# Kernel optimization log

Measured on AMD Instinct MI355X. Metric: run time of the kernel, lower is better.

Reference implementation:

```python
import jax, jax.numpy as jnp
import numpy as np
from jax import lax

M_DIM = 128
L1 = L2 = L3 = L4 = 4
L = L1 * L2 * L3 * L4  # 256
RANK = 2
BATCH, D = 4, 16
W = D - RANK + 1  # 15 windows per dim (linear mode, stride 1, drop)


def _make_bbasis():
    # Bbasis[idx, i] = prod_d cos(2*pi*(j_d+1)/(i+2)), idx = ((j1*L2+j2)*L3+j3)*L4+j4
    i = jnp.arange(M_DIM, dtype=jnp.float32)
    def c(Ld):
        j = jnp.arange(D_ := Ld, dtype=jnp.float32)
        return jnp.cos(2.0 * jnp.pi * (j[:, None] + 1.0) / (i[None, :] + 2.0))  # (Ld, m)
    B1, B2, B3, B4 = c(L1), c(L2), c(L3), c(L4)
    Bb = (B1[:, None, None, None, :] * B2[None, :, None, None, :]
          * B3[None, None, :, None, :] * B4[None, None, None, :, :])
    return Bb.reshape(L, M_DIM).astype(jnp.float32)


def setup_inputs() -> dict:
    key = jax.random.key(0)
    k1, k2, k3 = jax.random.split(key, 3)
    vec_arr = jax.random.normal(k1, (BATCH, D, D, D, D, M_DIM), dtype=jnp.float32)
    # M initialized as identity + small noise (nn.init.eye_ is exactly eye; noise keeps grads non-trivial)
    M = jnp.eye(M_DIM, dtype=jnp.float32) + 0.01 * jax.random.normal(k2, (M_DIM, M_DIM), dtype=jnp.float32)
    Acoeff = jax.random.uniform(k3, (M_DIM, L), minval=-0.1, maxval=0.1, dtype=jnp.float32)
    Bbasis = _make_bbasis()
    return {"vec_arr": vec_arr, "M": M, "Acoeff": Acoeff, "Bbasis": Bbasis}


def _basis_index():
    # window coords k_d in [0, W), basis index uses j_d = k_d mod L_d
    k = jnp.arange(W)
    j1 = (k % L1)[:, None, None, None]
    j2 = (k % L2)[None, :, None, None]
    j3 = (k % L3)[None, None, :, None]
    j4 = (k % L4)[None, None, None, :]
    idx = ((j1 * L2 + j2) * L3 + j3) * L4 + j4  # (W,W,W,W)
    return idx.reshape(-1)  # (W^4,)


def reference(vec_arr, M, Acoeff, Bbasis):
    # 4D sliding-window mean (linear mode, stride 1, 'drop'), rank_op='avg'.
    # mean(window @ M.T) == mean(window) @ M.T (linearity), so pool then one GEMM.
    win = (1, RANK, RANK, RANK, RANK, 1)
    pooled = lax.reduce_window(vec_arr, jnp.float32(0.0), lax.add, win,
                               (1, 1, 1, 1, 1, 1), 'VALID') / float(RANK ** 4)
    # agg[b, k1..k4, j] = sum_i pooled[...,i] * M[j,i]  (i.e. x @ M.T)
    agg = jnp.einsum('bwxyzi,ji->bwxyzj', pooled, M)  # (B, W,W,W,W, m)
    agg = agg.reshape(agg.shape[0], -1, M_DIM)        # (B, W^4, m)
    idx = _basis_index()                               # (W^4,)
    # Position-dependent descriptor N(k) = Acoeff[:, idx] * Bbasis[idx, :]
    Nk = Acoeff.T[idx] * Bbasis[idx]                   # (W^4, m)
    return Nk[None, :, :] - agg                        # (B, W^4, m) deviation
```

## Files before the change

kernel.cpp:

```cpp
#include <hip/hip_runtime.h>
#include <hip/hip_bf16.h>
#include <stdint.h>

#define MD     128
#define W4     50625
#define ROWS   202500
#define LBAS   256

#define P_ELEMS  27648000ull
#define P_BYTES  (P_ELEMS*2ull)
#define NK2_OFF  P_BYTES
#define MBF_OFF  (P_BYTES + 131072ull)
#define WS_NEED  (P_BYTES + 131072ull + 32768ull)

#define NK_OFF 51840000
#define POOL_THREADS 432000

typedef __attribute__((ext_vector_type(8))) __bf16 bf16x8;
typedef __attribute__((ext_vector_type(4))) float floatx4;
typedef __attribute__((ext_vector_type(8))) unsigned short ushortx8;
typedef __attribute__((ext_vector_type(4))) unsigned short ushortx4;

__device__ __forceinline__ float bf2f(unsigned short u){
  union { unsigned int i; float f; } v; v.i = ((unsigned int)u) << 16; return v.f;
}
__device__ __forceinline__ unsigned short f2bf(float x){
  union { float f; unsigned int i; } v; v.f = x;
  unsigned int r = v.i + 0x7FFFu + ((v.i >> 16) & 1u);
  return (unsigned short)(r >> 16);
}
__device__ __forceinline__ int detect_f32(const void* Bbasis){
  return ((const unsigned int*)Bbasis)[0] == 0x3F800000u;
}

__global__ __launch_bounds__(256) void nk2_kernel(const void* __restrict__ Acoeff,
                                                  const void* __restrict__ Bbasis,
                                                  const void* __restrict__ Mmat,
                                                  float* __restrict__ NkFull,
                                                  unsigned short* __restrict__ Mbf){
  int gid = blockIdx.x * 256 + threadIdx.x;
  const int isf = detect_f32(Bbasis);
  if (gid < LBAS * MD){
    int idx = gid >> 7, j = gid & 127;
    float a, b;
    if (isf){ a = ((const float*)Acoeff)[j*LBAS+idx]; b = ((const float*)Bbasis)[idx*MD+j]; }
    else    { a = bf2f(((const unsigned short*)Acoeff)[j*LBAS+idx]);
              b = bf2f(((const unsigned short*)Bbasis)[idx*MD+j]); }
    NkFull[gid] = a * b;
  } else {
    int m = gid - LBAS * MD;
    if (m < MD * MD){
      Mbf[m] = isf ? f2bf(((const float*)Mmat)[m]) : ((const unsigned short*)Mmat)[m];
    }
  }
}

__global__ __launch_bounds__(256) void passA_kernel(const void* __restrict__ vec,
                                                    const void* __restrict__ Bbasis,
                                                    unsigned short* __restrict__ P){
  __shared__ __align__(16) float S[256 * 68];

  const int bid = blockIdx.x;
  const int l   = (bid & 7) * 240 + (bid >> 3);
  const int w2  = l % 15;
  int r = l / 15;
  const int ih  = r & 1;  r >>= 1;
  const int x1  = r & 15;
  const int b   = r >> 4;
  const int t   = threadIdx.x;

  const size_t baseA = ((size_t)((b * 16 + x1) * 16 + w2)) * 32768 + (size_t)ih * 64;
  const size_t baseB = baseA + 32768;
  const int isf = detect_f32(Bbasis);

  if (isf){
    const float* vf = (const float*)vec;
#pragma unroll
    for (int k = 0; k < 16; ++k){
      const int e   = k * 1024 + t * 4;
      const size_t off = (size_t)(e >> 6) * 128 + (e & 63);
      const floatx4 a = *(const floatx4*)(vf + baseA + off);
      const floatx4 c = *(const floatx4*)(vf + baseB + off);
      floatx4 s;
#pragma unroll
      for (int q = 0; q < 4; ++q) s[q] = a[q] + c[q];
      *(floatx4*)&S[(e >> 6) * 68 + (e & 63)] = s;
    }
  } else {
    const unsigned short* vh = (const unsigned short*)vec;
#pragma unroll
    for (int k = 0; k < 16; ++k){
      const int e   = k * 1024 + t * 4;
      const size_t off = (size_t)(e >> 6) * 128 + (e & 63);
      const ushortx4 a = *(const ushortx4*)(vh + baseA + off);
      const ushortx4 c = *(const ushortx4*)(vh + baseB + off);
      floatx4 s;
#pragma unroll
      for (int q = 0; q < 4; ++q) s[q] = bf2f(a[q]) + bf2f(c[q]);
      *(floatx4*)&S[(e >> 6) * 68 + (e & 63)] = s;
    }
  }
  __syncthreads();

  const int ig = t & 7;
  const int wp = t >> 3;
  unsigned short* Pbase = P + ((size_t)((b * 16 + x1) * 15 + w2)) * 28800 + ih * 64 + ig * 8;
#pragma unroll
  for (int j = 0; j < 8; ++j){
    const int w34 = j * 32 + wp;
    if (w34 < 225){
      const int w3 = w34 / 15;
      const int w4 = w34 - w3 * 15;
      const int p00 = (w3 * 16 + w4) * 68 + ig * 8;
      const float* r00 = &S[p00];
      const float* r01 = &S[p00 + 68];
      const float* r10 = &S[p00 + 68 * 16];
      const float* r11 = &S[p00 + 68 * 17];
      ushortx8 ov;
#pragma unroll
      for (int e = 0; e < 8; ++e){
        const float s = (r00[e] + r01[e]) + (r10[e] + r11[e]);
        ov[e] = f2bf(s * 0.125f);
      }
      *(ushortx8*)(Pbase + (size_t)w34 * 128) = ov;
    }
  }
}

__global__ __launch_bounds__(256) void passB_kernel(const unsigned short* __restrict__ P,
                                                    const float* __restrict__ NkFull,
                                                    const unsigned short* __restrict__ Mbf,
                                                    const void* __restrict__ Bbasis,
                                                    void* __restrict__ out){
  __shared__ __align__(16) unsigned short sAp[128][136];
  __shared__ __align__(16) unsigned short sB[128][136];
  __shared__ __align__(16) float sNk[16 * 128];
  __shared__ unsigned char sJ[128];

  const int bid = blockIdx.x;
  const int l   = (bid % 8) * 225 + (bid / 8);
  const int half = l & 1;
  int s2 = l >> 1;
  const int w2 = s2 % 15;  s2 /= 15;
  const int w1 = s2 % 15;
  const int b  = s2 / 15;
  const int r0 = half * 128;
  const int RN = half ? 97 : 128;
  const int t  = threadIdx.x;
  const int isf = detect_f32(Bbasis);

  {
    const int rr  = t >> 4;
    const int l16 = t & 15;
    const size_t sb0 = ((size_t)((b * 16 + w1) * 15 + w2)) * 28800;
    const size_t sb1 = sb0 + 432000;
#pragma unroll
    for (int it = 0; it < 8; ++it){
      const int row = it * 16 + rr;
      const size_t off = (size_t)(r0 + row) * 128 + l16 * 8;
      const ushortx8 u0 = *(const ushortx8*)(P + sb0 + off);
      const ushortx8 u1 = *(const ushortx8*)(P + sb1 + off);
      ushortx8 sv;
#pragma unroll
      for (int e = 0; e < 8; ++e) sv[e] = f2bf((bf2f(u0[e]) + bf2f(u1[e])) * 0.5f);
      *(ushortx8*)&sAp[row][l16 * 8] = sv;
      *(ushortx8*)&sB[row][l16 * 8] = *(const ushortx8*)(Mbf + row * 128 + l16 * 8);
    }
  }
  {
    const int nkbase = ((w1 & 3) * 4 + (w2 & 3)) * 16;
    const floatx4 n0 = *(const floatx4*)(NkFull + nkbase * 128 + t * 8);
    const floatx4 n1 = *(const floatx4*)(NkFull + nkbase * 128 + t * 8 + 4);
    *(floatx4*)&sNk[t * 8]     = n0;
    *(floatx4*)&sNk[t * 8 + 4] = n1;
  }
  if (t < 128){
    const int w34 = r0 + t;
    if (w34 < 225){
      const int w3 = w34 / 15;
      const int w4 = w34 - w3 * 15;
      sJ[t] = (unsigned char)((w3 & 3) * 4 + (w4 & 3));
    } else sJ[t] = 0;
  }
  __syncthreads();

  const int wave = t >> 6;
  const int lane = t & 63;
  const int quad = lane >> 4;
  const int l16m = lane & 15;

  floatx4 acc[2][8];
#pragma unroll
  for (int rt = 0; rt < 2; ++rt)
#pragma unroll
    for (int c = 0; c < 8; ++c) acc[rt][c] = (floatx4){0.f, 0.f, 0.f, 0.f};

#pragma unroll
  for (int s = 0; s < 4; ++s){
    const bf16x8 af0 = *(const bf16x8*)&sAp[wave * 16 + l16m][s * 32 + quad * 8];
    const bf16x8 af1 = *(const bf16x8*)&sAp[64 + wave * 16 + l16m][s * 32 + quad * 8];
#pragma unroll
    for (int c = 0; c < 8; ++c){
      const bf16x8 bfv = *(const bf16x8*)&sB[c * 16 + l16m][s * 32 + quad * 8];
      acc[0][c] = __builtin_amdgcn_mfma_f32_16x16x32_bf16(af0, bfv, acc[0][c], 0, 0, 0);
      acc[1][c] = __builtin_amdgcn_mfma_f32_16x16x32_bf16(af1, bfv, acc[1][c], 0, 0, 0);
    }
  }
  __syncthreads();

  float* Ct = (float*)&sB[0][0];
  const size_t prow0 = ((size_t)((b * 15 + w1) * 15 + w2)) * 225 + r0;

#pragma unroll
  for (int s = 0; s < 2; ++s){
#pragma unroll
    for (int c = 0; c < 8; ++c)
#pragma unroll
      for (int reg = 0; reg < 4; ++reg)
        Ct[(wave * 16 + quad * 4 + reg) * 132 + c * 16 + l16m] = acc[s][c][reg];
    __syncthreads();

    const int col = (t & 31) * 4;
#pragma unroll
    for (int k = 0; k < 8; ++k){
      const int lr = k * 8 + (t >> 5);
      const int rloc = 64 * s + lr;
      if (rloc < RN){
        const floatx4 v  = *(const floatx4*)&Ct[lr * 132 + col];
        const floatx4 nk = *(const floatx4*)&sNk[(int)sJ[rloc] * 128 + col];
        floatx4 o;
#pragma unroll
        for (int e = 0; e < 4; ++e) o[e] = nk[e] - v[e];
        const size_t p = prow0 + rloc;
        if (isf){
          *(floatx4*)((float*)out + p * 128 + col) = o;
        } else {
          ushortx4 ob;
#pragma unroll
          for (int e = 0; e < 4; ++e) ob[e] = f2bf(o[e]);
          *(ushortx4*)((unsigned short*)out + p * 128 + col) = ob;
        }
      }
    }
    if (s == 0) __syncthreads();
  }
}

__global__ __launch_bounds__(256) void nk_kernel(const void* __restrict__ Acoeff,
                                                 const void* __restrict__ Bbasis,
                                                 float* __restrict__ NkFull){
  int gid = blockIdx.x * 256 + threadIdx.x;
  if (gid >= LBAS * MD) return;
  int idx = gid >> 7, j = gid & 127;
  float a, b;
  if (detect_f32(Bbasis)){
    a = ((const float*)Acoeff)[j * LBAS + idx];
    b = ((const float*)Bbasis)[idx * MD + j];
  } else {
    a = bf2f(((const unsigned short*)Acoeff)[j * LBAS + idx]);
    b = bf2f(((const unsigned short*)Bbasis)[idx * MD + j]);
  }
  NkFull[gid] = a * b;
}

template<int ISF32>
__device__ __forceinline__ void pool_body(const void* __restrict__ vec,
                                          unsigned short* __restrict__ pooled,
                                          int gid){
  const int ig = gid & 31;
  unsigned int strip = (unsigned int)(gid >> 5);
  const unsigned int w4 = strip % 15u; strip /= 15u;
  const unsigned int w3 = strip % 15u; strip /= 15u;
  const unsigned int w2 = strip % 15u;
  const unsigned int b  = strip / 15u;
  const unsigned int base = b*8388608u + w2*32768u + w3*2048u + w4*128u
                          + (unsigned int)(ig * 4);
  unsigned int offs[8];
#pragma unroll
  for (int d = 0; d < 8; ++d){
    const unsigned int d2 = (d>>2)&1u, d3 = (d>>1)&1u, d4 = d&1u;
    offs[d] = base + d2*32768u + d3*2048u + d4*128u;
  }
  const unsigned int prowB = b*50625u + w2*225u + w3*15u + w4;
  float prev[4], cur[4];
#pragma unroll 4
  for (int k1 = 0; k1 < 16; ++k1){
#pragma unroll
    for (int e = 0; e < 4; ++e) cur[e] = 0.f;
#pragma unroll
    for (int d = 0; d < 8; ++d){
      const unsigned int off = offs[d] + (unsigned int)k1 * 524288u;
      if (ISF32){
        const floatx4 v = *(const floatx4*)((const float*)vec + off);
#pragma unroll
        for (int e = 0; e < 4; ++e) cur[e] += v[e];
      } else {
        const ushortx4 u = *(const ushortx4*)((const unsigned short*)vec + off);
#pragma unroll
        for (int e = 0; e < 4; ++e) cur[e] += bf2f(u[e]);
      }
    }
    if (k1 > 0){
      ushortx4 ov;
#pragma unroll
      for (int e = 0; e < 4; ++e) ov[e] = f2bf((prev[e] + cur[e]) * 0.0625f);
      *(ushortx4*)(pooled + (size_t)(prowB + (unsigned)(k1 - 1) * 3375u) * 128 + ig * 4) = ov;
    }
#pragma unroll
    for (int e = 0; e < 4; ++e) prev[e] = cur[e];
  }
}

__global__ __launch_bounds__(256) void pool_kernel(const void* __restrict__ vec,
                                                   const void* __restrict__ Bbasis,
                                                   unsigned short* __restrict__ pooled){
  int gid = blockIdx.x * 256 + threadIdx.x;
  if (gid >= POOL_THREADS) return;
  if (detect_f32(Bbasis)) pool_body<1>(vec, pooled, gid);
  else                    pool_body<0>(vec, pooled, gid);
}

union GemmSmem {
  struct { unsigned short A[128][136]; unsigned short B[128][136]; } ab;
  float C[128][132];
};

__global__ __launch_bounds__(256) void gemm_kernel(const unsigned short* __restrict__ pooled,
                                                   const void* __restrict__ Mmat,
                                                   const float* __restrict__ NkFull,
                                                   const void* __restrict__ Bbasis,
                                                   void* __restrict__ out){
  __shared__ __align__(16) GemmSmem sm;
  __shared__ int sIdx[128];

  const int tid = threadIdx.x;
  const int p0  = blockIdx.x * 128;
  const int isF32 = detect_f32(Bbasis);

  {
    const int rr  = tid >> 4;
    const int l16 = tid & 15;
#pragma unroll
    for (int r8 = 0; r8 < 8; ++r8){
      const int row = r8 * 16 + rr;
      *(ushortx8*)&sm.ab.A[row][l16 * 8] =
          *(const ushortx8*)(pooled + (size_t)(p0 + row) * 128 + l16 * 8);
    }
    if (isF32){
      const float* mf = (const float*)Mmat;
#pragma unroll
      for (int r8 = 0; r8 < 8; ++r8){
        const int row = r8 * 16 + rr;
        const float* src = mf + row * 128 + l16 * 8;
        floatx4 lo = *(const floatx4*)src;
        floatx4 hi = *(const floatx4*)(src + 4);
        ushortx8 v;
#pragma unroll
        for (int e = 0; e < 4; ++e){ v[e] = f2bf(lo[e]); v[4+e] = f2bf(hi[e]); }
        *(ushortx8*)&sm.ab.B[row][l16 * 8] = v;
      }
    } else {
      const unsigned short* mh = (const unsigned short*)Mmat;
#pragma unroll
      for (int r8 = 0; r8 < 8; ++r8){
        const int row = r8 * 16 + rr;
        *(ushortx8*)&sm.ab.B[row][l16 * 8] = *(const ushortx8*)(mh + row * 128 + l16 * 8);
      }
    }
  }
  if (tid < 128){
    const int p = p0 + tid;
    unsigned int w = (p < ROWS) ? (unsigned int)(p % W4) : 0u;
    const unsigned int w4 = w % 15u; w /= 15u;
    const unsigned int w3 = w % 15u; w /= 15u;
    const unsigned int w2 = w % 15u;
    const unsigned int w1 = w / 15u;
    sIdx[tid] = (int)(((w1 & 3u) << 6) | ((w2 & 3u) << 4) | ((w3 & 3u) << 2) | (w4 & 3u));
  }
  __syncthreads();

  const int wave = tid >> 6;
  const int lane = tid & 63;
  const int quad = lane >> 4;
  const int l16  = lane & 15;

  floatx4 acc[2][8];
#pragma unroll
  for (int rt = 0; rt < 2; ++rt)
#pragma unroll
    for (int c = 0; c < 8; ++c) acc[rt][c] = (floatx4){0.f, 0.f, 0.f, 0.f};

#pragma unroll
  for (int s = 0; s < 4; ++s){
    bf16x8 af[2];
#pragma unroll
    for (int rt = 0; rt < 2; ++rt)
      af[rt] = *(const bf16x8*)&sm.ab.A[wave * 32 + rt * 16 + l16][s * 32 + quad * 8];
#pragma unroll
    for (int c = 0; c < 8; ++c){
      const bf16x8 bfv = *(const bf16x8*)&sm.ab.B[c * 16 + l16][s * 32 + quad * 8];
      acc[0][c] = __builtin_amdgcn_mfma_f32_16x16x32_bf16(af[0], bfv, acc[0][c], 0, 0, 0);
      acc[1][c] = __builtin_amdgcn_mfma_f32_16x16x32_bf16(af[1], bfv, acc[1][c], 0, 0, 0);
    }
  }

  __syncthreads();
#pragma unroll
  for (int rt = 0; rt < 2; ++rt){
#pragma unroll
    for (int c = 0; c < 8; ++c){
#pragma unroll
      for (int reg = 0; reg < 4; ++reg){
        const int r = wave * 32 + rt * 16 + quad * 4 + reg;
        sm.C[r][c * 16 + l16] = acc[rt][c][reg];
      }
    }
  }
  __syncthreads();

  const int rsub = tid >> 5;
  const int col  = (tid & 31) * 4;
#pragma unroll
  for (int k = 0; k < 16; ++k){
    const int row = k * 8 + rsub;
    const int p = p0 + row;
    if (p >= ROWS) continue;
    const floatx4 v = *(const floatx4*)&sm.C[row][col];
    const floatx4 nk = *(const floatx4*)(NkFull + (sIdx[row] << 7) + col);
    floatx4 o;
#pragma unroll
    for (int e = 0; e < 4; ++e) o[e] = nk[e] - v[e];
    if (isF32){
      *(floatx4*)((float*)out + (size_t)p * 128 + col) = o;
    } else {
      ushortx4 ob;
#pragma unroll
      for (int e = 0; e < 4; ++e) ob[e] = f2bf(o[e]);
      *(ushortx4*)((unsigned short*)out + (size_t)p * 128 + col) = ob;
    }
  }
}

extern "C" void kernel_launch(void* const* d_in, const int* in_sizes, int n_in,
                              void* d_out, int out_size, void* d_ws, size_t ws_size,
                              hipStream_t stream) {
  const void* vec = d_in[0];
  const void* Mm  = d_in[1];
  const void* Ac  = d_in[2];
  const void* Bb  = d_in[3];

  if (ws_size >= WS_NEED){
    unsigned short* P = (unsigned short*)d_ws;
    float* NkFull = (float*)((char*)d_ws + NK2_OFF);
    unsigned short* Mbf = (unsigned short*)((char*)d_ws + MBF_OFF);
    nk2_kernel<<<192, 256, 0, stream>>>(Ac, Bb, Mm, NkFull, Mbf);
    passA_kernel<<<1920, 256, 0, stream>>>(vec, Bb, P);
    passB_kernel<<<1800, 256, 0, stream>>>(P, NkFull, Mbf, Bb, d_out);
  } else {
    unsigned short* pooled = (unsigned short*)d_ws;
    float* NkFull = (float*)((char*)d_ws + NK_OFF);
    nk_kernel<<<128, 256, 0, stream>>>(Ac, Bb, NkFull);
    pool_kernel<<<(POOL_THREADS + 255) / 256, 256, 0, stream>>>(vec, Bb, pooled);
    gemm_kernel<<<(ROWS + 127) / 128, 256, 0, stream>>>(pooled, Mm, NkFull, Bb, d_out);
  }
}
```

Measured before the change: 267.9 us.

## Split passA and passB shared-memory staging into channel halves to raise occupancy

passA now stages 32 channels at a time in a smaller LDS buffer, processing two halves sequentially. The intermediate P layout changes to channel-quarter-major blocks of 32 channels. passB splits the K dimension into two 64-wide halves that share one smaller LDS buffer, and adds occupancy hints to launch_bounds. The aim is to cut LDS per block so more blocks fit per CU and memory latency is better hidden, at the cost of extra barriers and shorter contiguous global reads (64-byte segments).

Result: no change. 264.8 us (-1.2%).

```diff
diff --git a/kernel.cpp b/kernel.cpp
--- a/kernel.cpp
+++ b/kernel.cpp
@@ -55,10 +55,10 @@
   }
 }
 
-__global__ __launch_bounds__(256) void passA_kernel(const void* __restrict__ vec,
-                                                    const void* __restrict__ Bbasis,
-                                                    unsigned short* __restrict__ P){
-  __shared__ __align__(16) float S[256 * 68];
+__global__ __launch_bounds__(256, 4) void passA_kernel(const void* __restrict__ vec,
+                                                       const void* __restrict__ Bbasis,
+                                                       unsigned short* __restrict__ P){
+  __shared__ __align__(16) float S[256 * 36];
 
   const int bid = blockIdx.x;
   const int l   = (bid & 7) * 240 + (bid >> 3);
@@ -68,72 +68,80 @@
   const int x1  = r & 15;
   const int b   = r >> 4;
   const int t   = threadIdx.x;
-
-  const size_t baseA = ((size_t)((b * 16 + x1) * 16 + w2)) * 32768 + (size_t)ih * 64;
-  const size_t baseB = baseA + 32768;
   const int isf = detect_f32(Bbasis);
 
-  if (isf){
-    const float* vf = (const float*)vec;
-#pragma unroll
-    for (int k = 0; k < 16; ++k){
-      const int e   = k * 1024 + t * 4;
-      const size_t off = (size_t)(e >> 6) * 128 + (e & 63);
-      const floatx4 a = *(const floatx4*)(vf + baseA + off);
-      const floatx4 c = *(const floatx4*)(vf + baseB + off);
-      floatx4 s;
-#pragma unroll
-      for (int q = 0; q < 4; ++q) s[q] = a[q] + c[q];
-      *(floatx4*)&S[(e >> 6) * 68 + (e & 63)] = s;
-    }
-  } else {
-    const unsigned short* vh = (const unsigned short*)vec;
-#pragma unroll
-    for (int k = 0; k < 16; ++k){
-      const int e   = k * 1024 + t * 4;
-      const size_t off = (size_t)(e >> 6) * 128 + (e & 63);
-      const ushortx4 a = *(const ushortx4*)(vh + baseA + off);
-      const ushortx4 c = *(const ushortx4*)(vh + baseB + off);
-      floatx4 s;
-#pragma unroll
-      for (int q = 0; q < 4; ++q) s[q] = bf2f(a[q]) + bf2f(c[q]);
-      *(floatx4*)&S[(e >> 6) * 68 + (e & 63)] = s;
-    }
-  }
-  __syncthreads();
-
-  const int ig = t & 7;
-  const int wp = t >> 3;
-  unsigned short* Pbase = P + ((size_t)((b * 16 + x1) * 15 + w2)) * 28800 + ih * 64 + ig * 8;
-#pragma unroll
-  for (int j = 0; j < 8; ++j){
-    const int w34 = j * 32 + wp;
-    if (w34 < 225){
-      const int w3 = w34 / 15;
-      const int w4 = w34 - w3 * 15;
-      const int p00 = (w3 * 16 + w4) * 68 + ig * 8;
-      const float* r00 = &S[p00];
-      const float* r01 = &S[p00 + 68];
-      const float* r10 = &S[p00 + 68 * 16];
-      const float* r11 = &S[p00 + 68 * 17];
-      ushortx8 ov;
-#pragma unroll
-      for (int e = 0; e < 8; ++e){
-        const float s = (r00[e] + r01[e]) + (r10[e] + r11[e]);
-        ov[e] = f2bf(s * 0.125f);
-      }
-      *(ushortx8*)(Pbase + (size_t)w34 * 128) = ov;
-    }
-  }
-}
-
-__global__ __launch_bounds__(256) void passB_kernel(const unsigned short* __restrict__ P,
-                                                    const float* __restrict__ NkFull,
-                                                    const unsigned short* __restrict__ Mbf,
-                                                    const void* __restrict__ Bbasis,
-                                                    void* __restrict__ out){
-  __shared__ __align__(16) unsigned short sAp[128][136];
-  __shared__ __align__(16) unsigned short sB[128][136];
+  const size_t slab0 = ((size_t)((b * 16 + x1) * 16 + w2)) * 32768;
+  unsigned short* Pblk = P + ((size_t)((b * 16 + x1) * 15 + w2)) * 28800;
+
+#pragma unroll
+  for (int half = 0; half < 2; ++half){
+    const int chb = ih * 64 + half * 32;
+    if (half) __syncthreads();
+    if (isf){
+      const float* vf = (const float*)vec;
+#pragma unroll
+      for (int k = 0; k < 8; ++k){
+        const int f   = k * 256 + t;
+        const int row = f >> 3;
+        const int c4  = f & 7;
+        const size_t off = slab0 + (size_t)row * 128 + chb + c4 * 4;
+        const floatx4 a = *(const floatx4*)(vf + off);
+        const floatx4 c = *(const floatx4*)(vf + off + 32768);
+        floatx4 s;
+#pragma unroll
+        for (int q = 0; q < 4; ++q) s[q] = a[q] + c[q];
+        *(floatx4*)&S[row * 36 + c4 * 4] = s;
+      }
+    } else {
+      const unsigned short* vh = (const unsigned short*)vec;
+#pragma unroll
+      for (int k = 0; k < 4; ++k){
+        const int f   = k * 256 + t;
+        const int row = f >> 2;
+        const int c8  = f & 3;
+        const size_t off = slab0 + (size_t)row * 128 + chb + c8 * 8;
+        const ushortx8 a = *(const ushortx8*)(vh + off);
+        const ushortx8 c = *(const ushortx8*)(vh + off + 32768);
+        floatx4 s0, s1;
+#pragma unroll
+        for (int q = 0; q < 4; ++q){ s0[q] = bf2f(a[q]) + bf2f(c[q]);
+                                     s1[q] = bf2f(a[4+q]) + bf2f(c[4+q]); }
+        *(floatx4*)&S[row * 36 + c8 * 8]     = s0;
+        *(floatx4*)&S[row * 36 + c8 * 8 + 4] = s1;
+      }
+    }
+    __syncthreads();
+
+    unsigned short* Pdst = Pblk + (size_t)(ih * 2 + half) * 7200;
+#pragma unroll
+    for (int j = 0; j < 4; ++j){
+      const int o = j * 256 + t;
+      if (o < 900){
+        const int w34 = o >> 2;
+        const int c8  = (o & 3) * 8;
+        const int w3  = w34 / 15;
+        const int w4  = w34 - w3 * 15;
+        const int p00 = (w3 * 16 + w4) * 36 + c8;
+        const float* r00 = &S[p00];
+        const float* r01 = &S[p00 + 36];
+        const float* r10 = &S[p00 + 576];
+        const float* r11 = &S[p00 + 612];
+        ushortx8 ov;
+#pragma unroll
+        for (int e = 0; e < 8; ++e)
+          ov[e] = f2bf(((r00[e] + r01[e]) + (r10[e] + r11[e])) * 0.125f);
+        *(ushortx8*)(Pdst + (size_t)w34 * 32 + c8) = ov;
+      }
+    }
+  }
+}
+
+__global__ __launch_bounds__(256, 3) void passB_kernel(const unsigned short* __restrict__ P,
+                                                       const float* __restrict__ NkFull,
+                                                       const unsigned short* __restrict__ Mbf,
+                                                       const void* __restrict__ Bbasis,
+                                                       void* __restrict__ out){
+  __shared__ __align__(16) unsigned short sAB[2][128][72];
   __shared__ __align__(16) float sNk[16 * 128];
   __shared__ unsigned char sJ[128];
 
@@ -149,30 +157,13 @@
   const int t  = threadIdx.x;
   const int isf = detect_f32(Bbasis);
 
-  {
-    const int rr  = t >> 4;
-    const int l16 = t & 15;
-    const size_t sb0 = ((size_t)((b * 16 + w1) * 15 + w2)) * 28800;
-    const size_t sb1 = sb0 + 432000;
-#pragma unroll
-    for (int it = 0; it < 8; ++it){
-      const int row = it * 16 + rr;
-      const size_t off = (size_t)(r0 + row) * 128 + l16 * 8;
-      const ushortx8 u0 = *(const ushortx8*)(P + sb0 + off);
-      const ushortx8 u1 = *(const ushortx8*)(P + sb1 + off);
-      ushortx8 sv;
-#pragma unroll
-      for (int e = 0; e < 8; ++e) sv[e] = f2bf((bf2f(u0[e]) + bf2f(u1[e])) * 0.5f);
-      *(ushortx8*)&sAp[row][l16 * 8] = sv;
-      *(ushortx8*)&sB[row][l16 * 8] = *(const ushortx8*)(Mbf + row * 128 + l16 * 8);
-    }
-  }
+  const size_t sb0 = ((size_t)((b * 16 + w1) * 15 + w2)) * 28800;
+  const size_t sb1 = sb0 + 432000;
+
   {
     const int nkbase = ((w1 & 3) * 4 + (w2 & 3)) * 16;
-    const floatx4 n0 = *(const floatx4*)(NkFull + nkbase * 128 + t * 8);
-    const floatx4 n1 = *(const floatx4*)(NkFull + nkbase * 128 + t * 8 + 4);
-    *(floatx4*)&sNk[t * 8]     = n0;
-    *(floatx4*)&sNk[t * 8 + 4] = n1;
+    *(floatx4*)&sNk[t * 8]     = *(const floatx4*)(NkFull + nkbase * 128 + t * 8);
+    *(floatx4*)&sNk[t * 8 + 4] = *(const floatx4*)(NkFull + nkbase * 128 + t * 8 + 4);
   }
   if (t < 128){
     const int w34 = r0 + t;
@@ -182,7 +173,6 @@
       sJ[t] = (unsigned char)((w3 & 3) * 4 + (w4 & 3));
     } else sJ[t] = 0;
   }
-  __syncthreads();
 
   const int wave = t >> 6;
   const int lane = t & 63;
@@ -195,20 +185,45 @@
 #pragma unroll
     for (int c = 0; c < 8; ++c) acc[rt][c] = (floatx4){0.f, 0.f, 0.f, 0.f};
 
-#pragma unroll
-  for (int s = 0; s < 4; ++s){
-    const bf16x8 af0 = *(const bf16x8*)&sAp[wave * 16 + l16m][s * 32 + quad * 8];
-    const bf16x8 af1 = *(const bf16x8*)&sAp[64 + wave * 16 + l16m][s * 32 + quad * 8];
-#pragma unroll
-    for (int c = 0; c < 8; ++c){
-      const bf16x8 bfv = *(const bf16x8*)&sB[c * 16 + l16m][s * 32 + quad * 8];
-      acc[0][c] = __builtin_amdgcn_mfma_f32_16x16x32_bf16(af0, bfv, acc[0][c], 0, 0, 0);
-      acc[1][c] = __builtin_amdgcn_mfma_f32_16x16x32_bf16(af1, bfv, acc[1][c], 0, 0, 0);
+  const int l8 = t & 7;
+  const int rr = t >> 3;
+
+#pragma unroll
+  for (int kh = 0; kh < 2; ++kh){
+    if (kh) __syncthreads();
+    const int chq = kh * 2 + (l8 >> 2);
+    const int cw  = (l8 & 3) * 8;
+#pragma unroll
+    for (int it = 0; it < 4; ++it){
+      const int row  = it * 32 + rr;
+      const int rowg = (r0 + row < 225) ? (r0 + row) : 224;
+      const size_t off = (size_t)chq * 7200 + (size_t)rowg * 32 + cw;
+      const ushortx8 u0 = *(const ushortx8*)(P + sb0 + off);
+      const ushortx8 u1 = *(const ushortx8*)(P + sb1 + off);
+      ushortx8 sv;
+#pragma unroll
+      for (int e = 0; e < 8; ++e) sv[e] = f2bf((bf2f(u0[e]) + bf2f(u1[e])) * 0.5f);
+      *(ushortx8*)&sAB[0][row][l8 * 8] = sv;
+      *(ushortx8*)&sAB[1][row][l8 * 8] =
+          *(const ushortx8*)(Mbf + row * 128 + kh * 64 + l8 * 8);
+    }
+    __syncthreads();
+
+#pragma unroll
+    for (int s = 0; s < 2; ++s){
+      const bf16x8 af0 = *(const bf16x8*)&sAB[0][wave * 16 + l16m][s * 32 + quad * 8];
+      const bf16x8 af1 = *(const bf16x8*)&sAB[0][64 + wave * 16 + l16m][s * 32 + quad * 8];
+#pragma unroll
+      for (int c = 0; c < 8; ++c){
+        const bf16x8 bfv = *(const bf16x8*)&sAB[1][c * 16 + l16m][s * 32 + quad * 8];
+        acc[0][c] = __builtin_amdgcn_mfma_f32_16x16x32_bf16(af0, bfv, acc[0][c], 0, 0, 0);
+        acc[1][c] = __builtin_amdgcn_mfma_f32_16x16x32_bf16(af1, bfv, acc[1][c], 0, 0, 0);
+      }
     }
   }
   __syncthreads();
 
-  float* Ct = (float*)&sB[0][0];
+  float* Ct = (float*)&sAB[0][0][0];
   const size_t prow0 = ((size_t)((b * 15 + w1) * 15 + w2)) * 225 + r0;
 
 #pragma unroll
```
